# Kernel tuning notes

Hardware: AMD Instinct MI355X
Metric: run time of the kernel (lower is better)

The kernel has to match this reference:

```python
import jax, jax.numpy as jnp
import numpy as np

B, S, D, H = 2, 2048, 1024, 16
DH = D // H  # 64


def setup_inputs() -> dict:
    key = jax.random.key(0)
    ks = jax.random.split(key, 7)
    scale = 0.02
    return {
        "q": jax.random.normal(ks[0], (B, S, D), dtype=jnp.float32),
        "k": jax.random.normal(ks[1], (B, S, D), dtype=jnp.float32),
        "v": jax.random.normal(ks[2], (B, S, D), dtype=jnp.float32),
        "Wq": jax.random.normal(ks[3], (D, D), dtype=jnp.float32) * scale,
        "Wk": jax.random.normal(ks[4], (D, D), dtype=jnp.float32) * scale,
        "Wv": jax.random.normal(ks[5], (D, D), dtype=jnp.float32) * scale,
        "Wo": jax.random.normal(ks[6], (D, D), dtype=jnp.float32) * scale,
    }


def _split_heads(x):
    # [B, S, D] -> [B, H, S, DH]
    b, s, d = x.shape
    return x.reshape(b, s, H, DH).transpose(0, 2, 1, 3)


def reference(q, k, v, Wq, Wk, Wv, Wo):
    # Linear projections (torch Linear: x @ W.T, bias=False)
    qh = _split_heads(q @ Wq.T)  # [B, H, S, DH]
    kh = _split_heads(k @ Wk.T)
    vh = _split_heads(v @ Wv.T)
    # Scaled dot-product attention (manual, materializes scores as original)
    scores = jnp.einsum("bhqd,bhkd->bhqk", qh, kh) / jnp.sqrt(
        jnp.asarray(DH, dtype=qh.dtype)
    )  # [B, H, S, S]
    attn = jax.nn.softmax(scores, axis=-1)
    out = jnp.einsum("bhqk,bhkd->bhqd", attn, vh)  # [B, H, S, DH]
    # Concat heads: [B, H, S, DH] -> [B, S, D]
    out = out.transpose(0, 2, 1, 3).reshape(q.shape[0], q.shape[1], D)
    return out @ Wo.T
```

## Files before the change

kernel.cpp:

```cpp
#include <hip/hip_runtime.h>
#include <hip/hip_bf16.h>
#include <math.h>

namespace {
constexpr int Hn  = 16;
constexpr int DH  = 64;
constexpr int S   = 2048;
constexpr int D   = 1024;
constexpr int B   = 2;
constexpr int N   = B * S;
}

typedef __attribute__((ext_vector_type(8))) short bf16x8;
typedef __attribute__((ext_vector_type(4))) float f32x4;

#if defined(__has_builtin)
#if __has_builtin(__builtin_amdgcn_exp2f)
#define HAVE_EXP2_BUILTIN 1
#endif
#endif

static __device__ __forceinline__ float exp2_fast(float x) {
#ifdef HAVE_EXP2_BUILTIN
    return __builtin_amdgcn_exp2f(x);
#else
    float r;
    asm("v_exp_f32 %0, %1" : "=v"(r) : "v"(x));
    return r;
#endif
}

static __device__ __forceinline__ ushort bf16rd(float x) {
    unsigned u = __builtin_bit_cast(unsigned, x);
    return (ushort)((u + 0x8000u) >> 16);
}
static __device__ __forceinline__ float bfu2f(ushort h) {
    unsigned u = (unsigned)h << 16;
    return __builtin_bit_cast(float, u);
}
static __device__ __forceinline__ void split1(float a, ushort& h, ushort& l) {
    h = bf16rd(a);
    l = bf16rd(a - bfu2f(h));
}

static __device__ __forceinline__ void gload16(const ushort* g, ushort* l) {
    __builtin_amdgcn_global_load_lds((const unsigned int*)g, (unsigned int*)l, 16, 0, 0);
}

__global__ __launch_bounds__(256) void split_all(
    const float4* __restrict__ q, const float4* __restrict__ k, const float4* __restrict__ v,
    const float4* __restrict__ wq, const float4* __restrict__ wk,
    const float4* __restrict__ wv, const float4* __restrict__ wo,
    ushort4* __restrict__ qh, ushort4* __restrict__ kh, ushort4* __restrict__ vh,
    ushort4* __restrict__ wqh, ushort4* __restrict__ wkh, ushort4* __restrict__ wvh,
    ushort4* __restrict__ woh, ushort4* __restrict__ wol,
    int n4a, int n4w) {
    const int total = 3 * n4a + 4 * n4w;
    const int stride = gridDim.x * 256;
    for (int i = blockIdx.x * 256 + threadIdx.x; i < total; i += stride) {
        if (i < 3 * n4a) {
            const int which = i / n4a;
            const int j = i - which * n4a;
            const float4 val = (which == 0 ? q : which == 1 ? k : v)[j];
            ushort4* ph = which == 0 ? qh : which == 1 ? kh : vh;
            ph[j] = make_ushort4(bf16rd(val.x), bf16rd(val.y), bf16rd(val.z), bf16rd(val.w));
        } else {
            const int t = i - 3 * n4a;
            const int which = t / n4w;
            const int j = t - which * n4w;
            const float4 val = (which == 0 ? wq : which == 1 ? wk : which == 2 ? wv : wo)[j];
            if (which == 3) {
                ushort4 hh, ll;
                split1(val.x, hh.x, ll.x);
                split1(val.y, hh.y, ll.y);
                split1(val.z, hh.z, ll.z);
                split1(val.w, hh.w, ll.w);
                woh[j] = hh;
                wol[j] = ll;
            } else {
                ushort4* ph = which == 0 ? wqh : which == 1 ? wkh : wvh;
                ph[j] = make_ushort4(bf16rd(val.x), bf16rd(val.y), bf16rd(val.z), bf16rd(val.w));
            }
        }
    }
}

__global__ __launch_bounds__(256) void gemm_qkv(
    const ushort* __restrict__ qbf, const ushort* __restrict__ kbf,
    const ushort* __restrict__ vbf,
    const ushort* __restrict__ Wqh, const ushort* __restrict__ Wkh,
    const ushort* __restrict__ Wvh,
    ushort* __restrict__ Qbh, ushort* __restrict__ Kbh,
    ushort* __restrict__ Vtb, float qscale) {
    constexpr int BK = 64;
    constexpr int K = D;
    __shared__ __align__(16) ushort sA[128 * BK];
    __shared__ __align__(16) ushort sB[128 * BK];

    const int tid = threadIdx.x;
    const int which = blockIdx.y >> 3;
    const int m0 = blockIdx.x * 128;
    const int n0 = (blockIdx.y & 7) * 128;

    const ushort* A = which == 0 ? qbf : which == 1 ? kbf : vbf;
    const ushort* W = which == 0 ? Wqh : which == 1 ? Wkh : Wvh;

    const int l  = tid & 63;
    const int w  = tid >> 6;
    const int wm = w >> 1, wn = w & 1;
    const int lm = l & 15, g = l >> 4;

    const int srow = l >> 3;
    const int schunk = (l & 7) ^ srow;
    const ushort* gA = A + (size_t)(m0 + w * 32 + srow) * K + schunk * 8;
    const ushort* gB = W + (size_t)(n0 + w * 32 + srow) * K + schunk * 8;
    ushort* lA = &sA[(w * 32) * BK];
    ushort* lB = &sB[(w * 32) * BK];

    const f32x4 fzero = {0.f, 0.f, 0.f, 0.f};
    f32x4 acc[4][4];
#pragma unroll
    for (int mi = 0; mi < 4; ++mi)
#pragma unroll
        for (int ni = 0; ni < 4; ++ni) acc[mi][ni] = fzero;

    const int rsw = lm & 7;

    for (int s = 0; s < K / BK; ++s) {
        const int k0 = s * BK;
        if (s) __syncthreads();
#pragma unroll
        for (int j = 0; j < 4; ++j) {
            gload16(gA + (size_t)(j * 8) * K + k0, lA + (j * 8) * BK);
            gload16(gB + (size_t)(j * 8) * K + k0, lB + (j * 8) * BK);
        }
        __syncthreads();

#pragma unroll
        for (int kk = 0; kk < 2; ++kk) {
            bf16x8 ah[4], bh[4];
#pragma unroll
            for (int mi = 0; mi < 4; ++mi)
                ah[mi] = *(const bf16x8*)&sA[(wm * 64 + mi * 16 + lm) * BK + (((kk * 4 + g) ^ rsw) * 8)];
#pragma unroll
            for (int ni = 0; ni < 4; ++ni)
                bh[ni] = *(const bf16x8*)&sB[(wn * 64 + ni * 16 + lm) * BK + (((kk * 4 + g) ^ rsw) * 8)];
            __builtin_amdgcn_s_setprio(1);
#pragma unroll
            for (int mi = 0; mi < 4; ++mi)
#pragma unroll
                for (int ni = 0; ni < 4; ++ni)
                    acc[mi][ni] = __builtin_amdgcn_mfma_f32_16x16x32_bf16(
                        ah[mi], bh[ni], acc[mi][ni], 0, 0, 0);
            __builtin_amdgcn_s_setprio(0);
        }
    }

#pragma unroll
    for (int mi = 0; mi < 4; ++mi)
#pragma unroll
        for (int ni = 0; ni < 4; ++ni) {
            const int col = n0 + wn * 64 + ni * 16 + lm;
            const int rbase = m0 + wm * 64 + mi * 16 + g * 4;
            const int hh = col >> 6, dh = col & (DH - 1);
            if (which == 0) {
#pragma unroll
                for (int r = 0; r < 4; ++r) {
                    const int row = rbase + r;
                    const int bb = row >> 11, ss = row & (S - 1);
                    const size_t idx = (((size_t)(bb * Hn + hh)) * S + ss) * DH + dh;
                    Qbh[idx] = bf16rd(acc[mi][ni][r] * qscale);
                }
            } else if (which == 1) {
#pragma unroll
                for (int r = 0; r < 4; ++r) {
                    const int row = rbase + r;
                    const int bb = row >> 11, ss = row & (S - 1);
                    const size_t idx = (((size_t)(bb * Hn + hh)) * S + ss) * DH + dh;
                    Kbh[idx] = bf16rd(acc[mi][ni][r]);
                }
            } else {
                const int bb = rbase >> 11, ss = rbase & (S - 1);
                ushort4 pk;
                pk.x = bf16rd(acc[mi][ni][0]);
                pk.y = bf16rd(acc[mi][ni][1]);
                pk.z = bf16rd(acc[mi][ni][2]);
                pk.w = bf16rd(acc[mi][ni][3]);
                const size_t idx = (((size_t)(bb * Hn + hh)) * DH + dh) * S + ss;
                *(ushort4*)&Vtb[idx] = pk;
            }
        }
}

__global__ __launch_bounds__(256) void gemm_out(const ushort* __restrict__ Ah,
                                                const ushort* __restrict__ Al,
                                                const ushort* __restrict__ Wh,
                                                const ushort* __restrict__ Wl,
                                                float* __restrict__ C) {
    constexpr int BK = 32;
    constexpr int LDT = 40;
    constexpr int K = D, O = D;
    __shared__ __align__(16) ushort sAh[2][128 * LDT];
    __shared__ __align__(16) ushort sAl[2][128 * LDT];
    __shared__ __align__(16) ushort sBh[2][64 * LDT];
    __shared__ __align__(16) ushort sBl[2][64 * LDT];

    const int tid = threadIdx.x;
    const int m0 = blockIdx.x * 128;
    const int n0 = blockIdx.y * 64;

    const int l   = tid & 63;
    const int wid = tid >> 6;
    const int wm  = wid >> 1;
    const int wn  = wid & 1;
    const int lm  = l & 15;
    const int g   = l >> 4;
    const int lk  = g * 8;

    const int arow0 = tid >> 2;
    const int aslot = (tid & 3) * 8;
    const ushort* gAh0 = Ah + (size_t)(m0 + arow0) * K + aslot;
    const ushort* gAh1 = gAh0 + (size_t)64 * K;
    const ushort* gAl0 = Al + (size_t)(m0 + arow0) * K + aslot;
    const ushort* gAl1 = gAl0 + (size_t)64 * K;
    const ushort* gBh  = Wh + (size_t)(n0 + arow0) * K + aslot;
    const ushort* gBl  = Wl + (size_t)(n0 + arow0) * K + aslot;

    const f32x4 fzero = {0.f, 0.f, 0.f, 0.f};
    f32x4 acc[4][2];
#pragma unroll
    for (int mi = 0; mi < 4; ++mi)
#pragma unroll
        for (int ni = 0; ni < 2; ++ni) acc[mi][ni] = fzero;

    uint4 rA0 = *(const uint4*)gAh0, rA1 = *(const uint4*)gAh1;
    uint4 rA2 = *(const uint4*)gAl0, rA3 = *(const uint4*)gAl1;
    uint4 rB0 = *(const uint4*)gBh,  rB1 = *(const uint4*)gBl;

    *(uint4*)&sAh[0][arow0 * LDT + aslot]        = rA0;
    *(uint4*)&sAh[0][(arow0 + 64) * LDT + aslot] = rA1;
    *(uint4*)&sAl[0][arow0 * LDT + aslot]        = rA2;
    *(uint4*)&sAl[0][(arow0 + 64) * LDT + aslot] = rA3;
    *(uint4*)&sBh[0][arow0 * LDT + aslot]        = rB0;
    *(uint4*)&sBl[0][arow0 * LDT + aslot]        = rB1;
    rA0 = *(const uint4*)(gAh0 + BK); rA1 = *(const uint4*)(gAh1 + BK);
    rA2 = *(const uint4*)(gAl0 + BK); rA3 = *(const uint4*)(gAl1 + BK);
    rB0 = *(const uint4*)(gBh + BK);  rB1 = *(const uint4*)(gBl + BK);
    __syncthreads();

    constexpr int NS = K / BK;
    int cur = 0;
    for (int s = 0; s < NS; ++s) {
        bf16x8 ah[4], al[4], bh[2], bl[2];
#pragma unroll
        for (int mi = 0; mi < 4; ++mi) {
            const int row = wm * 64 + mi * 16 + lm;
            ah[mi] = *(const bf16x8*)&sAh[cur][row * LDT + lk];
            al[mi] = *(const bf16x8*)&sAl[cur][row * LDT + lk];
        }
#pragma unroll
        for (int ni = 0; ni < 2; ++ni) {
            const int rowb = wn * 32 + ni * 16 + lm;
            bh[ni] = *(const bf16x8*)&sBh[cur][rowb * LDT + lk];
            bl[ni] = *(const bf16x8*)&sBl[cur][rowb * LDT + lk];
        }
        __builtin_amdgcn_s_setprio(1);
#pragma unroll
        for (int mi = 0; mi < 4; ++mi)
#pragma unroll
            for (int ni = 0; ni < 2; ++ni) {
                acc[mi][ni] = __builtin_amdgcn_mfma_f32_16x16x32_bf16(
                    al[mi], bh[ni], acc[mi][ni], 0, 0, 0);
                acc[mi][ni] = __builtin_amdgcn_mfma_f32_16x16x32_bf16(
                    ah[mi], bl[ni], acc[mi][ni], 0, 0, 0);
                acc[mi][ni] = __builtin_amdgcn_mfma_f32_16x16x32_bf16(
                    ah[mi], bh[ni], acc[mi][ni], 0, 0, 0);
            }
        __builtin_amdgcn_s_setprio(0);

        if (s < NS - 1) {
            const int nx = cur ^ 1;
            *(uint4*)&sAh[nx][arow0 * LDT + aslot]        = rA0;
            *(uint4*)&sAh[nx][(arow0 + 64) * LDT + aslot] = rA1;
            *(uint4*)&sAl[nx][arow0 * LDT + aslot]        = rA2;
            *(uint4*)&sAl[nx][(arow0 + 64) * LDT + aslot] = rA3;
            *(uint4*)&sBh[nx][arow0 * LDT + aslot]        = rB0;
            *(uint4*)&sBl[nx][arow0 * LDT + aslot]        = rB1;
            if (s < NS - 2) {
                const int kn = (s + 2) * BK;
                rA0 = *(const uint4*)(gAh0 + kn); rA1 = *(const uint4*)(gAh1 + kn);
                rA2 = *(const uint4*)(gAl0 + kn); rA3 = *(const uint4*)(gAl1 + kn);
                rB0 = *(const uint4*)(gBh + kn);  rB1 = *(const uint4*)(gBl + kn);
            }
            __syncthreads();
            cur = nx;
        }
    }

#pragma unroll
    for (int mi = 0; mi < 4; ++mi)
#pragma unroll
        for (int ni = 0; ni < 2; ++ni) {
            const int col = n0 + wn * 32 + ni * 16 + lm;
            const int rbase = m0 + wm * 64 + mi * 16 + g * 4;
#pragma unroll
            for (int r = 0; r < 4; ++r)
                C[(size_t)(rbase + r) * O + col] = acc[mi][ni][r];
        }
}

__global__ __launch_bounds__(256) void attn_mfma(const ushort* __restrict__ Qbh,
                                                 const ushort* __restrict__ Kbh,
                                                 const ushort* __restrict__ Vt,
                                                 ushort* __restrict__ AOh,
                                                 ushort* __restrict__ AOl) {
    constexpr int LDT = 72;
    __shared__ __align__(16) ushort Ksh[2][64 * LDT];
    __shared__ __align__(16) ushort Vts[2][64 * LDT];
    __shared__ __align__(16) ushort Ps[128 * LDT];

    const int tid = threadIdx.x;
    const int l = tid & 63, w = tid >> 6;
    const int g = l >> 4, l15 = l & 15;
    const int bh = blockIdx.x;
    const int q0 = blockIdx.y * 128;
    const size_t bhb = (size_t)bh * S * DH;

    bf16x8 qh_[2][2];
#pragma unroll
    for (int qb = 0; qb < 2; ++qb)
#pragma unroll
        for (int kk = 0; kk < 2; ++kk) {
            const size_t idx = bhb + (size_t)(q0 + w * 32 + qb * 16 + l15) * DH + kk * 32 + g * 8;
            qh_[qb][kk] = *(const bf16x8*)(Qbh + idx);
        }

    const int r_st = tid >> 2;
    const int c0 = (tid & 3) * 16;
    const ushort* gKh = Kbh + bhb + (size_t)r_st * DH + c0;
    const ushort* gVt = Vt + (size_t)bh * DH * S + (size_t)r_st * S + c0;

    uint4 pk0 = *(const uint4*)gKh, pk1 = *(const uint4*)(gKh + 8);
    uint4 pv0 = *(const uint4*)gVt, pv1 = *(const uint4*)(gVt + 8);

    const f32x4 fzero = {0.f, 0.f, 0.f, 0.f};
    f32x4 o_acc[2][4];
    f32x4 l_acc[2];
#pragma unroll
    for (int qb = 0; qb < 2; ++qb) {
        l_acc[qb] = fzero;
#pragma unroll
        for (int f = 0; f < 4; ++f) o_acc[qb][f] = fzero;
    }

    bf16x8 ones;
#pragma unroll
    for (int i = 0; i < 8; ++i) ones[i] = (short)0x3F80;

    *(uint4*)&Ksh[0][r_st * LDT + c0]     = pk0;
    *(uint4*)&Ksh[0][r_st * LDT + c0 + 8] = pk1;
    *(uint4*)&Vts[0][r_st * LDT + c0]     = pv0;
    *(uint4*)&Vts[0][r_st * LDT + c0 + 8] = pv1;
    pk0 = *(const uint4*)(gKh + 64 * DH); pk1 = *(const uint4*)(gKh + 64 * DH + 8);
    pv0 = *(const uint4*)(gVt + 64);      pv1 = *(const uint4*)(gVt + 64 + 8);
    __syncthreads();

    constexpr int NT = S / 64;
    int cur = 0;
    for (int kt = 0; kt < NT; ++kt) {
        f32x4 sc[2][4];
#pragma unroll
        for (int qb = 0; qb < 2; ++qb)
#pragma unroll
            for (int f = 0; f < 4; ++f) sc[qb][f] = fzero;
#pragma unroll
        for (int kk = 0; kk < 2; ++kk) {
            bf16x8 kh[4];
#pragma unroll
            for (int f = 0; f < 4; ++f)
                kh[f] = *(const bf16x8*)&Ksh[cur][(f * 16 + l15) * LDT + kk * 32 + g * 8];
            __builtin_amdgcn_s_setprio(1);
#pragma unroll
            for (int f = 0; f < 4; ++f)
#pragma unroll
                for (int qb = 0; qb < 2; ++qb)
                    sc[qb][f] = __builtin_amdgcn_mfma_f32_16x16x32_bf16(
                        qh_[qb][kk], kh[f], sc[qb][f], 0, 0, 0);
            __builtin_amdgcn_s_setprio(0);
        }

#pragma unroll
        for (int qb = 0; qb < 2; ++qb)
#pragma unroll
            for (int f = 0; f < 4; ++f) {
#pragma unroll
                for (int r = 0; r < 4; ++r) {
                    const int prow = w * 32 + qb * 16 + g * 4 + r;
                    const int chunk = (f * 2 + (l15 >> 3)) ^ ((prow >> 2) & 7);
                    Ps[prow * LDT + chunk * 8 + (l15 & 7)] =
                        bf16rd(exp2_fast(sc[qb][f][r]));
                }
            }

#pragma unroll
        for (int kk = 0; kk < 2; ++kk) {
            const int row0 = w * 32 + l15;
            const int row1 = row0 + 16;
            const int ck = kk * 4 + g;
            const bf16x8 pa0 = *(const bf16x8*)&Ps[row0 * LDT + ((ck ^ ((row0 >> 2) & 7)) * 8)];
            const bf16x8 pa1 = *(const bf16x8*)&Ps[row1 * LDT + ((ck ^ ((row1 >> 2) & 7)) * 8)];
            __builtin_amdgcn_s_setprio(1);
            l_acc[0] = __builtin_amdgcn_mfma_f32_16x16x32_bf16(pa0, ones, l_acc[0], 0, 0, 0);
            l_acc[1] = __builtin_amdgcn_mfma_f32_16x16x32_bf16(pa1, ones, l_acc[1], 0, 0, 0);
#pragma unroll
            for (int f = 0; f < 4; ++f) {
                const bf16x8 vt = *(const bf16x8*)&Vts[cur][(f * 16 + l15) * LDT + kk * 32 + g * 8];
                o_acc[0][f] = __builtin_amdgcn_mfma_f32_16x16x32_bf16(pa0, vt, o_acc[0][f], 0, 0, 0);
                o_acc[1][f] = __builtin_amdgcn_mfma_f32_16x16x32_bf16(pa1, vt, o_acc[1][f], 0, 0, 0);
            }
            __builtin_amdgcn_s_setprio(0);
        }

        if (kt < NT - 1) {
            const int nx = cur ^ 1;
            *(uint4*)&Ksh[nx][r_st * LDT + c0]     = pk0;
            *(uint4*)&Ksh[nx][r_st * LDT + c0 + 8] = pk1;
            *(uint4*)&Vts[nx][r_st * LDT + c0]     = pv0;
            *(uint4*)&Vts[nx][r_st * LDT + c0 + 8] = pv1;
            if (kt < NT - 2) {
                const int ok = (kt + 2) * 64 * DH;
                const int ov = (kt + 2) * 64;
                pk0 = *(const uint4*)(gKh + ok); pk1 = *(const uint4*)(gKh + ok + 8);
                pv0 = *(const uint4*)(gVt + ov); pv1 = *(const uint4*)(gVt + ov + 8);
            }
            __syncthreads();
            cur = nx;
        }
    }

    const int bb = bh >> 4, hh = bh & 15;
#pragma unroll
    for (int qb = 0; qb < 2; ++qb)
#pragma unroll
        for (int r = 0; r < 4; ++r) {
            const float inv = 1.f / l_acc[qb][r];
            const int row = q0 + w * 32 + qb * 16 + g * 4 + r;
#pragma unroll
            for (int f = 0; f < 4; ++f) {
                const float val = o_acc[qb][f][r] * inv;
                const size_t idx = ((size_t)(bb * S + row)) * D + hh * DH + f * 16 + l15;
                ushort hi, lo;
                split1(val, hi, lo);
                AOh[idx] = hi;
                AOl[idx] = lo;
            }
        }
}

extern "C" void kernel_launch(void* const* d_in, const int* in_sizes, int n_in,
                              void* d_out, int out_size, void* d_ws, size_t ws_size,
                              hipStream_t stream) {
    (void)in_sizes; (void)n_in; (void)out_size; (void)ws_size;
    const float* q  = (const float*)d_in[0];
    const float* k  = (const float*)d_in[1];
    const float* v  = (const float*)d_in[2];
    const float* Wq = (const float*)d_in[3];
    const float* Wk = (const float*)d_in[4];
    const float* Wv = (const float*)d_in[5];
    const float* Wo = (const float*)d_in[6];
    float* out = (float*)d_out;

    uint8_t* w8 = (uint8_t*)d_ws;
    constexpr size_t MB = 1u << 20;
    ushort* Wqh = (ushort*)(w8 + 0 * MB);
    ushort* Wkh = (ushort*)(w8 + 2 * MB);
    ushort* Wvh = (ushort*)(w8 + 4 * MB);
    ushort* Woh = (ushort*)(w8 + 6 * MB);
    ushort* Wol = (ushort*)(w8 + 8 * MB);
    ushort* qbf = (ushort*)(w8 + 16 * MB);
    ushort* kbf = (ushort*)(w8 + 24 * MB);
    ushort* vbf = (ushort*)(w8 + 32 * MB);
    ushort* Qbh = (ushort*)(w8 + 40 * MB);
    ushort* Kbh = (ushort*)(w8 + 48 * MB);
    ushort* Vtb = (ushort*)(w8 + 56 * MB);
    ushort* AOh = (ushort*)(w8 + 64 * MB);
    ushort* AOl = (ushort*)(w8 + 72 * MB);

    const int n4_act = (N * D) / 4;
    const int n4_w   = (D * D) / 4;
    const dim3 blk(256);

    split_all<<<2048, blk, 0, stream>>>(
        (const float4*)q, (const float4*)k, (const float4*)v,
        (const float4*)Wq, (const float4*)Wk, (const float4*)Wv, (const float4*)Wo,
        (ushort4*)qbf, (ushort4*)kbf, (ushort4*)vbf,
        (ushort4*)Wqh, (ushort4*)Wkh, (ushort4*)Wvh,
        (ushort4*)Woh, (ushort4*)Wol,
        n4_act, n4_w);

    const float qscale = 0.125f * 1.4426950408889634f;
    gemm_qkv<<<dim3(N / 128, 24), blk, 0, stream>>>(
        qbf, kbf, vbf, Wqh, Wkh, Wvh, Qbh, Kbh, Vtb, qscale);

    attn_mfma<<<dim3(B * Hn, S / 128), blk, 0, stream>>>(
        Qbh, Kbh, Vtb, AOh, AOl);

    gemm_out<<<dim3(N / 128, D / 64), blk, 0, stream>>>(AOh, AOl, Woh, Wol, out);
}
```

Before: 149.9 us.

## Vectorize GEMM epilogue stores via swapped MFMA operands and hoist attention LDS staging

```diff
diff --git a/kernel.cpp b/kernel.cpp
--- a/kernel.cpp
+++ b/kernel.cpp
@@ -34,6 +34,9 @@
     unsigned u = __builtin_bit_cast(unsigned, x);
     return (ushort)((u + 0x8000u) >> 16);
 }
+static __device__ __forceinline__ ushort bf16tr(float x) {
+    return (ushort)(__builtin_bit_cast(unsigned, x) >> 16);
+}
 static __device__ __forceinline__ float bfu2f(ushort h) {
     unsigned u = (unsigned)h << 16;
     return __builtin_bit_cast(float, u);
@@ -41,10 +44,6 @@
 static __device__ __forceinline__ void split1(float a, ushort& h, ushort& l) {
     h = bf16rd(a);
     l = bf16rd(a - bfu2f(h));
-}
-
-static __device__ __forceinline__ void gload16(const ushort* g, ushort* l) {
-    __builtin_amdgcn_global_load_lds((const unsigned int*)g, (unsigned int*)l, 16, 0, 0);
 }
 
 __global__ __launch_bounds__(256) void split_all(
@@ -85,6 +84,10 @@
     }
 }
 
+static __device__ __forceinline__ void gload16(const ushort* g, ushort* l) {
+    __builtin_amdgcn_global_load_lds((const unsigned int*)g, (unsigned int*)l, 16, 0, 0);
+}
+
 __global__ __launch_bounds__(256) void gemm_qkv(
     const ushort* __restrict__ qbf, const ushort* __restrict__ kbf,
     const ushort* __restrict__ vbf,
@@ -146,12 +149,21 @@
             for (int ni = 0; ni < 4; ++ni)
                 bh[ni] = *(const bf16x8*)&sB[(wn * 64 + ni * 16 + lm) * BK + (((kk * 4 + g) ^ rsw) * 8)];
             __builtin_amdgcn_s_setprio(1);
-#pragma unroll
-            for (int mi = 0; mi < 4; ++mi)
-#pragma unroll
-                for (int ni = 0; ni < 4; ++ni)
-                    acc[mi][ni] = __builtin_amdgcn_mfma_f32_16x16x32_bf16(
-                        ah[mi], bh[ni], acc[mi][ni], 0, 0, 0);
+            if (which < 2) {
+#pragma unroll
+                for (int mi = 0; mi < 4; ++mi)
+#pragma unroll
+                    for (int ni = 0; ni < 4; ++ni)
+                        acc[mi][ni] = __builtin_amdgcn_mfma_f32_16x16x32_bf16(
+                            bh[ni], ah[mi], acc[mi][ni], 0, 0, 0);
+            } else {
+#pragma unroll
+                for (int mi = 0; mi < 4; ++mi)
+#pragma unroll
+                    for (int ni = 0; ni < 4; ++ni)
+                        acc[mi][ni] = __builtin_amdgcn_mfma_f32_16x16x32_bf16(
+                            ah[mi], bh[ni], acc[mi][ni], 0, 0, 0);
+            }
             __builtin_amdgcn_s_setprio(0);
         }
     }
@@ -160,26 +172,24 @@
     for (int mi = 0; mi < 4; ++mi)
 #pragma unroll
         for (int ni = 0; ni < 4; ++ni) {
-            const int col = n0 + wn * 64 + ni * 16 + lm;
-            const int rbase = m0 + wm * 64 + mi * 16 + g * 4;
-            const int hh = col >> 6, dh = col & (DH - 1);
-            if (which == 0) {
-#pragma unroll
-                for (int r = 0; r < 4; ++r) {
-                    const int row = rbase + r;
-                    const int bb = row >> 11, ss = row & (S - 1);
-                    const size_t idx = (((size_t)(bb * Hn + hh)) * S + ss) * DH + dh;
-                    Qbh[idx] = bf16rd(acc[mi][ni][r] * qscale);
-                }
-            } else if (which == 1) {
-#pragma unroll
-                for (int r = 0; r < 4; ++r) {
-                    const int row = rbase + r;
-                    const int bb = row >> 11, ss = row & (S - 1);
-                    const size_t idx = (((size_t)(bb * Hn + hh)) * S + ss) * DH + dh;
-                    Kbh[idx] = bf16rd(acc[mi][ni][r]);
-                }
+            if (which < 2) {
+                const int arow = m0 + wm * 64 + mi * 16 + lm;
+                const int obase = n0 + wn * 64 + ni * 16 + g * 4;
+                const int bb = arow >> 11, ss = arow & (S - 1);
+                const int hh = obase >> 6, dh = obase & (DH - 1);
+                const float sc_ = which == 0 ? qscale : 1.0f;
+                ushort4 pk;
+                pk.x = bf16rd(acc[mi][ni][0] * sc_);
+                pk.y = bf16rd(acc[mi][ni][1] * sc_);
+                pk.z = bf16rd(acc[mi][ni][2] * sc_);
+                pk.w = bf16rd(acc[mi][ni][3] * sc_);
+                ushort* dst = which == 0 ? Qbh : Kbh;
+                const size_t idx = (((size_t)(bb * Hn + hh)) * S + ss) * DH + dh;
+                *(ushort4*)&dst[idx] = pk;
             } else {
+                const int col = n0 + wn * 64 + ni * 16 + lm;
+                const int rbase = m0 + wm * 64 + mi * 16 + g * 4;
+                const int hh = col >> 6, dh = col & (DH - 1);
                 const int bb = rbase >> 11, ss = rbase & (S - 1);
                 ushort4 pk;
                 pk.x = bf16rd(acc[mi][ni][0]);
@@ -270,11 +280,11 @@
 #pragma unroll
             for (int ni = 0; ni < 2; ++ni) {
                 acc[mi][ni] = __builtin_amdgcn_mfma_f32_16x16x32_bf16(
-                    al[mi], bh[ni], acc[mi][ni], 0, 0, 0);
+                    bh[ni], al[mi], acc[mi][ni], 0, 0, 0);
                 acc[mi][ni] = __builtin_amdgcn_mfma_f32_16x16x32_bf16(
-                    ah[mi], bl[ni], acc[mi][ni], 0, 0, 0);
+                    bl[ni], ah[mi], acc[mi][ni], 0, 0, 0);
                 acc[mi][ni] = __builtin_amdgcn_mfma_f32_16x16x32_bf16(
-                    ah[mi], bh[ni], acc[mi][ni], 0, 0, 0);
+                    bh[ni], ah[mi], acc[mi][ni], 0, 0, 0);
             }
         __builtin_amdgcn_s_setprio(0);
 
@@ -301,11 +311,11 @@
     for (int mi = 0; mi < 4; ++mi)
 #pragma unroll
         for (int ni = 0; ni < 2; ++ni) {
-            const int col = n0 + wn * 32 + ni * 16 + lm;
-            const int rbase = m0 + wm * 64 + mi * 16 + g * 4;
-#pragma unroll
-            for (int r = 0; r < 4; ++r)
-                C[(size_t)(rbase + r) * O + col] = acc[mi][ni][r];
+            const int row = m0 + wm * 64 + mi * 16 + lm;
+            const int ob  = n0 + wn * 32 + ni * 16 + g * 4;
+            const float4 v = make_float4(acc[mi][ni][0], acc[mi][ni][1],
+                                         acc[mi][ni][2], acc[mi][ni][3]);
+            *(float4*)&C[(size_t)row * O + ob] = v;
         }
 }
 
@@ -368,59 +378,6 @@
     constexpr int NT = S / 64;
     int cur = 0;
     for (int kt = 0; kt < NT; ++kt) {
-        f32x4 sc[2][4];
-#pragma unroll
-        for (int qb = 0; qb < 2; ++qb)
-#pragma unroll
-            for (int f = 0; f < 4; ++f) sc[qb][f] = fzero;
-#pragma unroll
-        for (int kk = 0; kk < 2; ++kk) {
-            bf16x8 kh[4];
-#pragma unroll
-            for (int f = 0; f < 4; ++f)
-                kh[f] = *(const bf16x8*)&Ksh[cur][(f * 16 + l15) * LDT + kk * 32 + g * 8];
-            __builtin_amdgcn_s_setprio(1);
-#pragma unroll
-            for (int f = 0; f < 4; ++f)
-#pragma unroll
-                for (int qb = 0; qb < 2; ++qb)
-                    sc[qb][f] = __builtin_amdgcn_mfma_f32_16x16x32_bf16(
-                        qh_[qb][kk], kh[f], sc[qb][f], 0, 0, 0);
-            __builtin_amdgcn_s_setprio(0);
-        }
-
-#pragma unroll
-        for (int qb = 0; qb < 2; ++qb)
-#pragma unroll
-            for (int f = 0; f < 4; ++f) {
-#pragma unroll
-                for (int r = 0; r < 4; ++r) {
-                    const int prow = w * 32 + qb * 16 + g * 4 + r;
-                    const int chunk = (f * 2 + (l15 >> 3)) ^ ((prow >> 2) & 7);
-                    Ps[prow * LDT + chunk * 8 + (l15 & 7)] =
-                        bf16rd(exp2_fast(sc[qb][f][r]));
-                }
-            }
-
-#pragma unroll
-        for (int kk = 0; kk < 2; ++kk) {
-            const int row0 = w * 32 + l15;
-            const int row1 = row0 + 16;
-            const int ck = kk * 4 + g;
-            const bf16x8 pa0 = *(const bf16x8*)&Ps[row0 * LDT + ((ck ^ ((row0 >> 2) & 7)) * 8)];
-            const bf16x8 pa1 = *(const bf16x8*)&Ps[row1 * LDT + ((ck ^ ((row1 >> 2) & 7)) * 8)];
-            __builtin_amdgcn_s_setprio(1);
-            l_acc[0] = __builtin_amdgcn_mfma_f32_16x16x32_bf16(pa0, ones, l_acc[0], 0, 0, 0);
-            l_acc[1] = __builtin_amdgcn_mfma_f32_16x16x32_bf16(pa1, ones, l_acc[1], 0, 0, 0);
-#pragma unroll
-            for (int f = 0; f < 4; ++f) {
-                const bf16x8 vt = *(const bf16x8*)&Vts[cur][(f * 16 + l15) * LDT + kk * 32 + g * 8];
-                o_acc[0][f] = __builtin_amdgcn_mfma_f32_16x16x32_bf16(pa0, vt, o_acc[0][f], 0, 0, 0);
-                o_acc[1][f] = __builtin_amdgcn_mfma_f32_16x16x32_bf16(pa1, vt, o_acc[1][f], 0, 0, 0);
-            }
-            __builtin_amdgcn_s_setprio(0);
-        }
-
         if (kt < NT - 1) {
             const int nx = cur ^ 1;
             *(uint4*)&Ksh[nx][r_st * LDT + c0]     = pk0;
@@ -433,8 +390,64 @@
                 pk0 = *(const uint4*)(gKh + ok); pk1 = *(const uint4*)(gKh + ok + 8);
                 pv0 = *(const uint4*)(gVt + ov); pv1 = *(const uint4*)(gVt + ov + 8);
             }
+        }
+
+        f32x4 sc[2][4];
+#pragma unroll
+        for (int qb = 0; qb < 2; ++qb)
+#pragma unroll
+            for (int f = 0; f < 4; ++f) sc[qb][f] = fzero;
+#pragma unroll
+        for (int kk = 0; kk < 2; ++kk) {
+            bf16x8 kh[4];
+#pragma unroll
+            for (int f = 0; f < 4; ++f)
+                kh[f] = *(const bf16x8*)&Ksh[cur][(f * 16 + l15) * LDT + kk * 32 + g * 8];
+            __builtin_amdgcn_s_setprio(1);
+#pragma unroll
+            for (int f = 0; f < 4; ++f)
+#pragma unroll
+                for (int qb = 0; qb < 2; ++qb)
+                    sc[qb][f] = __builtin_amdgcn_mfma_f32_16x16x32_bf16(
+                        qh_[qb][kk], kh[f], sc[qb][f], 0, 0, 0);
+            __builtin_amdgcn_s_setprio(0);
+        }
+
+#pragma unroll
+        for (int qb = 0; qb < 2; ++qb)
+#pragma unroll
+            for (int f = 0; f < 4; ++f) {
+#pragma unroll
+                for (int r = 0; r < 4; ++r) {
+                    const int prow = w * 32 + qb * 16 + g * 4 + r;
+                    const int chunk = (f * 2 + (l15 >> 3)) ^ ((prow >> 2) & 7);
+                    Ps[prow * LDT + chunk * 8 + (l15 & 7)] =
+                        bf16tr(exp2_fast(sc[qb][f][r]));
+                }
+            }
+
+#pragma unroll
+        for (int kk = 0; kk < 2; ++kk) {
+            const int row0 = w * 32 + l15;
+            const int row1 = row0 + 16;
+            const int ck = kk * 4 + g;
+            const bf16x8 pa0 = *(const bf16x8*)&Ps[row0 * LDT + ((ck ^ ((row0 >> 2) & 7)) * 8)];
+            const bf16x8 pa1 = *(const bf16x8*)&Ps[row1 * LDT + ((ck ^ ((row1 >> 2) & 7)) * 8)];
+            __builtin_amdgcn_s_setprio(1);
+            l_acc[0] = __builtin_amdgcn_mfma_f32_16x16x32_bf16(pa0, ones, l_acc[0], 0, 0, 0);
+            l_acc[1] = __builtin_amdgcn_mfma_f32_16x16x32_bf16(pa1, ones, l_acc[1], 0, 0, 0);
+#pragma unroll
+            for (int f = 0; f < 4; ++f) {
+                const bf16x8 vt = *(const bf16x8*)&Vts[cur][(f * 16 + l15) * LDT + kk * 32 + g * 8];
+                o_acc[0][f] = __builtin_amdgcn_mfma_f32_16x16x32_bf16(pa0, vt, o_acc[0][f], 0, 0, 0);
+                o_acc[1][f] = __builtin_amdgcn_mfma_f32_16x16x32_bf16(pa1, vt, o_acc[1][f], 0, 0, 0);
+            }
+            __builtin_amdgcn_s_setprio(0);
+        }
+
+        if (kt < NT - 1) {
             __syncthreads();
-            cur = nx;
+            cur ^= 1;
         }
     }
 
```

New measurement: 161.7 us. +7.9%, slower.

## Split attention KV sequence across two wave groups and combine partial outputs

Applied to the files above, without the earlier changes.

```diff
diff --git a/kernel.cpp b/kernel.cpp
--- a/kernel.cpp
+++ b/kernel.cpp
@@ -33,6 +33,9 @@
 static __device__ __forceinline__ ushort bf16rd(float x) {
     unsigned u = __builtin_bit_cast(unsigned, x);
     return (ushort)((u + 0x8000u) >> 16);
+}
+static __device__ __forceinline__ ushort bf16tr(float x) {
+    return (ushort)(__builtin_bit_cast(unsigned, x) >> 16);
 }
 static __device__ __forceinline__ float bfu2f(ushort h) {
     unsigned u = (unsigned)h << 16;
@@ -309,18 +312,19 @@
         }
 }
 
-__global__ __launch_bounds__(256) void attn_mfma(const ushort* __restrict__ Qbh,
+__global__ __launch_bounds__(512) void attn_mfma(const ushort* __restrict__ Qbh,
                                                  const ushort* __restrict__ Kbh,
                                                  const ushort* __restrict__ Vt,
                                                  ushort* __restrict__ AOh,
                                                  ushort* __restrict__ AOl) {
     constexpr int LDT = 72;
-    __shared__ __align__(16) ushort Ksh[2][64 * LDT];
-    __shared__ __align__(16) ushort Vts[2][64 * LDT];
-    __shared__ __align__(16) ushort Ps[128 * LDT];
+    __shared__ __align__(16) ushort Ks[2][64 * LDT];
+    __shared__ __align__(16) ushort Vs[2][64 * LDT];
+    __shared__ __align__(16) ushort Ps[8][32 * LDT];
 
     const int tid = threadIdx.x;
     const int l = tid & 63, w = tid >> 6;
+    const int wq = w & 3, grp = w >> 2;
     const int g = l >> 4, l15 = l & 15;
     const int bh = blockIdx.x;
     const int q0 = blockIdx.y * 128;
@@ -331,17 +335,15 @@
     for (int qb = 0; qb < 2; ++qb)
 #pragma unroll
         for (int kk = 0; kk < 2; ++kk) {
-            const size_t idx = bhb + (size_t)(q0 + w * 32 + qb * 16 + l15) * DH + kk * 32 + g * 8;
+            const size_t idx = bhb + (size_t)(q0 + wq * 32 + qb * 16 + l15) * DH + kk * 32 + g * 8;
             qh_[qb][kk] = *(const bf16x8*)(Qbh + idx);
         }
 
-    const int r_st = tid >> 2;
-    const int c0 = (tid & 3) * 16;
+    const int t8 = tid & 255;
+    const int r_st = t8 >> 2;
+    const int c0 = (t8 & 3) * 16;
     const ushort* gKh = Kbh + bhb + (size_t)r_st * DH + c0;
     const ushort* gVt = Vt + (size_t)bh * DH * S + (size_t)r_st * S + c0;
-
-    uint4 pk0 = *(const uint4*)gKh, pk1 = *(const uint4*)(gKh + 8);
-    uint4 pv0 = *(const uint4*)gVt, pv1 = *(const uint4*)(gVt + 8);
 
     const f32x4 fzero = {0.f, 0.f, 0.f, 0.f};
     f32x4 o_acc[2][4];
@@ -357,17 +359,23 @@
 #pragma unroll
     for (int i = 0; i < 8; ++i) ones[i] = (short)0x3F80;
 
-    *(uint4*)&Ksh[0][r_st * LDT + c0]     = pk0;
-    *(uint4*)&Ksh[0][r_st * LDT + c0 + 8] = pk1;
-    *(uint4*)&Vts[0][r_st * LDT + c0]     = pv0;
-    *(uint4*)&Vts[0][r_st * LDT + c0 + 8] = pv1;
-    pk0 = *(const uint4*)(gKh + 64 * DH); pk1 = *(const uint4*)(gKh + 64 * DH + 8);
-    pv0 = *(const uint4*)(gVt + 64);      pv1 = *(const uint4*)(gVt + 64 + 8);
+    uint4 pk0, pk1, pv0, pv1;
+    {
+        const size_t ok = (size_t)grp * 64 * DH, ov = (size_t)grp * 64;
+        pk0 = *(const uint4*)(gKh + ok); pk1 = *(const uint4*)(gKh + ok + 8);
+        pv0 = *(const uint4*)(gVt + ov); pv1 = *(const uint4*)(gVt + ov + 8);
+        *(uint4*)&Ks[grp][r_st * LDT + c0]     = pk0;
+        *(uint4*)&Ks[grp][r_st * LDT + c0 + 8] = pk1;
+        *(uint4*)&Vs[grp][r_st * LDT + c0]     = pv0;
+        *(uint4*)&Vs[grp][r_st * LDT + c0 + 8] = pv1;
+        const size_t ok2 = (size_t)(2 + grp) * 64 * DH, ov2 = (size_t)(2 + grp) * 64;
+        pk0 = *(const uint4*)(gKh + ok2); pk1 = *(const uint4*)(gKh + ok2 + 8);
+        pv0 = *(const uint4*)(gVt + ov2); pv1 = *(const uint4*)(gVt + ov2 + 8);
+    }
     __syncthreads();
 
-    constexpr int NT = S / 64;
-    int cur = 0;
-    for (int kt = 0; kt < NT; ++kt) {
+    constexpr int NSI = S / 128;
+    for (int t = 0; t < NSI; ++t) {
         f32x4 sc[2][4];
 #pragma unroll
         for (int qb = 0; qb < 2; ++qb)
@@ -378,7 +386,7 @@
             bf16x8 kh[4];
 #pragma unroll
             for (int f = 0; f < 4; ++f)
-                kh[f] = *(const bf16x8*)&Ksh[cur][(f * 16 + l15) * LDT + kk * 32 + g * 8];
+                kh[f] = *(const bf16x8*)&Ks[grp][(f * 16 + l15) * LDT + kk * 32 + g * 8];
             __builtin_amdgcn_s_setprio(1);
 #pragma unroll
             for (int f = 0; f < 4; ++f)
@@ -395,66 +403,85 @@
             for (int f = 0; f < 4; ++f) {
 #pragma unroll
                 for (int r = 0; r < 4; ++r) {
-                    const int prow = w * 32 + qb * 16 + g * 4 + r;
+                    const int prow = qb * 16 + g * 4 + r;
                     const int chunk = (f * 2 + (l15 >> 3)) ^ ((prow >> 2) & 7);
-                    Ps[prow * LDT + chunk * 8 + (l15 & 7)] =
-                        bf16rd(exp2_fast(sc[qb][f][r]));
+                    Ps[w][prow * LDT + chunk * 8 + (l15 & 7)] =
+                        bf16tr(exp2_fast(sc[qb][f][r]));
                 }
             }
 
 #pragma unroll
         for (int kk = 0; kk < 2; ++kk) {
-            const int row0 = w * 32 + l15;
-            const int row1 = row0 + 16;
+            const int row0 = l15;
+            const int row1 = 16 + l15;
             const int ck = kk * 4 + g;
-            const bf16x8 pa0 = *(const bf16x8*)&Ps[row0 * LDT + ((ck ^ ((row0 >> 2) & 7)) * 8)];
-            const bf16x8 pa1 = *(const bf16x8*)&Ps[row1 * LDT + ((ck ^ ((row1 >> 2) & 7)) * 8)];
+            const bf16x8 pa0 = *(const bf16x8*)&Ps[w][row0 * LDT + ((ck ^ ((row0 >> 2) & 7)) * 8)];
+            const bf16x8 pa1 = *(const bf16x8*)&Ps[w][row1 * LDT + ((ck ^ ((row1 >> 2) & 7)) * 8)];
             __builtin_amdgcn_s_setprio(1);
             l_acc[0] = __builtin_amdgcn_mfma_f32_16x16x32_bf16(pa0, ones, l_acc[0], 0, 0, 0);
             l_acc[1] = __builtin_amdgcn_mfma_f32_16x16x32_bf16(pa1, ones, l_acc[1], 0, 0, 0);
 #pragma unroll
             for (int f = 0; f < 4; ++f) {
-                const bf16x8 vt = *(const bf16x8*)&Vts[cur][(f * 16 + l15) * LDT + kk * 32 + g * 8];
+                const bf16x8 vt = *(const bf16x8*)&Vs[grp][(f * 16 + l15) * LDT + kk * 32 + g * 8];
                 o_acc[0][f] = __builtin_amdgcn_mfma_f32_16x16x32_bf16(pa0, vt, o_acc[0][f], 0, 0, 0);
                 o_acc[1][f] = __builtin_amdgcn_mfma_f32_16x16x32_bf16(pa1, vt, o_acc[1][f], 0, 0, 0);
             }
             __builtin_amdgcn_s_setprio(0);
         }
 
-        if (kt < NT - 1) {
-            const int nx = cur ^ 1;
-            *(uint4*)&Ksh[nx][r_st * LDT + c0]     = pk0;
-            *(uint4*)&Ksh[nx][r_st * LDT + c0 + 8] = pk1;
-            *(uint4*)&Vts[nx][r_st * LDT + c0]     = pv0;
-            *(uint4*)&Vts[nx][r_st * LDT + c0 + 8] = pv1;
-            if (kt < NT - 2) {
-                const int ok = (kt + 2) * 64 * DH;
-                const int ov = (kt + 2) * 64;
+        __syncthreads();
+        if (t < NSI - 1) {
+            *(uint4*)&Ks[grp][r_st * LDT + c0]     = pk0;
+            *(uint4*)&Ks[grp][r_st * LDT + c0 + 8] = pk1;
+            *(uint4*)&Vs[grp][r_st * LDT + c0]     = pv0;
+            *(uint4*)&Vs[grp][r_st * LDT + c0 + 8] = pv1;
+            if (t < NSI - 2) {
+                const size_t ok = (size_t)(2 * (t + 2) + grp) * 64 * DH;
+                const size_t ov = (size_t)(2 * (t + 2) + grp) * 64;
                 pk0 = *(const uint4*)(gKh + ok); pk1 = *(const uint4*)(gKh + ok + 8);
                 pv0 = *(const uint4*)(gVt + ov); pv1 = *(const uint4*)(gVt + ov + 8);
             }
             __syncthreads();
-            cur = nx;
-        }
-    }
-
-    const int bb = bh >> 4, hh = bh & 15;
-#pragma unroll
-    for (int qb = 0; qb < 2; ++qb)
-#pragma unroll
-        for (int r = 0; r < 4; ++r) {
-            const float inv = 1.f / l_acc[qb][r];
-            const int row = q0 + w * 32 + qb * 16 + g * 4 + r;
-#pragma unroll
-            for (int f = 0; f < 4; ++f) {
-                const float val = o_acc[qb][f][r] * inv;
-                const size_t idx = ((size_t)(bb * S + row)) * D + hh * DH + f * 16 + l15;
-                ushort hi, lo;
-                split1(val, hi, lo);
-                AOh[idx] = hi;
-                AOl[idx] = lo;
-            }
-        }
+        }
+    }
+
+    float* comb  = (float*)&Ps[0][0];
+    float* lcomb = (float*)&Ks[0][0];
+    if (grp == 1) {
+#pragma unroll
+        for (int qb = 0; qb < 2; ++qb)
+#pragma unroll
+            for (int r = 0; r < 4; ++r) {
+                const int row = qb * 16 + g * 4 + r;
+#pragma unroll
+                for (int f = 0; f < 4; ++f)
+                    comb[wq * 2048 + row * 64 + f * 16 + l15] = o_acc[qb][f][r];
+                if (l15 == 0) lcomb[wq * 32 + row] = l_acc[qb][r];
+            }
+    }
+    __syncthreads();
+    if (grp == 0) {
+        const int bb = bh >> 4, hh = bh & 15;
+#pragma unroll
+        for (int qb = 0; qb < 2; ++qb)
+#pragma unroll
+            for (int r = 0; r < 4; ++r) {
+                const int row = qb * 16 + g * 4 + r;
+                const float lsum = l_acc[qb][r] + lcomb[wq * 32 + row];
+                const float inv = 1.f / lsum;
+                const int srow = q0 + wq * 32 + row;
+#pragma unroll
+                for (int f = 0; f < 4; ++f) {
+                    const float val =
+                        (o_acc[qb][f][r] + comb[wq * 2048 + row * 64 + f * 16 + l15]) * inv;
+                    const size_t idx = ((size_t)(bb * S + srow)) * D + hh * DH + f * 16 + l15;
+                    ushort hi, lo;
+                    split1(val, hi, lo);
+                    AOh[idx] = hi;
+                    AOl[idx] = lo;
+                }
+            }
+    }
 }
 
 extern "C" void kernel_launch(void* const* d_in, const int* in_sizes, int n_in,
@@ -502,7 +529,7 @@
     gemm_qkv<<<dim3(N / 128, 24), blk, 0, stream>>>(
         qbf, kbf, vbf, Wqh, Wkh, Wvh, Qbh, Kbh, Vtb, qscale);
 
-    attn_mfma<<<dim3(B * Hn, S / 128), blk, 0, stream>>>(
+    attn_mfma<<<dim3(B * Hn, S / 128), dim3(512), 0, stream>>>(
         Qbh, Kbh, Vtb, AOh, AOl);
 
     gemm_out<<<dim3(N / 128, D / 64), blk, 0, stream>>>(AOh, AOl, Woh, Wol, out);
```

Result: faster. 146.4 us (-2.3%).
